# Kernel optimization log

Hardware: AMD Instinct MI355X
Metric: run time of the kernel (lower is better)

Reference implementation:

```python
import jax, jax.numpy as jnp
import numpy as np

N_NODES = 524288
N_EDGES = 2097152
B = 16384
CONCAT = 128 + 128 + 881  # 1137


def _glorot(key, shape):
    fan_in, fan_out = shape[0], shape[1]
    s = jnp.sqrt(6.0 / (fan_in + fan_out))
    return jax.random.uniform(key, shape, jnp.float32, -s, s)


def setup_inputs() -> dict:
    key = jax.random.key(0)
    ks = jax.random.split(key, 24)
    inp = {
        'drug_x': jax.random.normal(ks[0], (N_NODES, 30), jnp.float32),
        'edge_index': jax.random.randint(ks[1], (2, N_EDGES), 0, N_NODES, jnp.int32),
        'batch': jnp.sort(jax.random.randint(ks[2], (N_NODES,), 0, B, jnp.int32)),
        'protein_x': jax.random.normal(ks[3], (B, 979), jnp.float32),
        'fppubchem': jax.random.uniform(ks[4], (B, 881), jnp.float32),
        # GCN layers (PyG GCNConv: linear no-bias, bias added after aggregation)
        'W1': _glorot(ks[5], (30, 64)), 'b1': jnp.zeros((64,), jnp.float32),
        'W2': _glorot(ks[6], (64, 64)), 'b2': jnp.zeros((64,), jnp.float32),
        'W3': _glorot(ks[7], (64, 64)), 'b3': jnp.zeros((64,), jnp.float32),
        'fc_drug_w': _glorot(ks[8], (64, 128)), 'fc_drug_b': jnp.zeros((128,), jnp.float32),
        'fc_prot_w': _glorot(ks[9], (979, 128)), 'fc_prot_b': jnp.zeros((128,), jnp.float32),
        'fc1_w': _glorot(ks[10], (CONCAT, 512)), 'fc1_b': jnp.zeros((512,), jnp.float32),
        'fc2_w': _glorot(ks[11], (512, 256)), 'fc2_b': jnp.zeros((256,), jnp.float32),
        'fc3_w': _glorot(ks[12], (256, 1)), 'fc3_b': jnp.zeros((1,), jnp.float32),
    }
    return inp


def _gcn_layer(x, W, b, src, dst, deg_inv_sqrt, n_nodes):
    # x' = D^-1/2 (A+I) D^-1/2 (x W) + b   (src/dst already include self-loops)
    h = x @ W
    norm = deg_inv_sqrt[src] * deg_inv_sqrt[dst]  # [E+N]
    msg = h[src] * norm[:, None]
    out = jax.ops.segment_sum(msg, dst, num_segments=n_nodes)
    return out + b


def reference(drug_x, edge_index, batch, protein_x, fppubchem,
              W1, b1, W2, b2, W3, b3,
              fc_drug_w, fc_drug_b, fc_prot_w, fc_prot_b,
              fc1_w, fc1_b, fc2_w, fc2_b, fc3_w, fc3_b):
    n = drug_x.shape[0]
    loops = jnp.arange(n, dtype=edge_index.dtype)
    src = jnp.concatenate([edge_index[0], loops])
    dst = jnp.concatenate([edge_index[1], loops])
    deg = jax.ops.segment_sum(jnp.ones_like(src, jnp.float32), dst, num_segments=n)
    deg_inv_sqrt = jnp.where(deg > 0, jax.lax.rsqrt(jnp.maximum(deg, 1.0)), 0.0)

    h = jax.nn.relu(_gcn_layer(drug_x, W1, b1, src, dst, deg_inv_sqrt, n))
    h = jax.nn.relu(_gcn_layer(h, W2, b2, src, dst, deg_inv_sqrt, n))
    h = jax.nn.relu(_gcn_layer(h, W3, b3, src, dst, deg_inv_sqrt, n))

    # global mean pool over graphs
    nb = fppubchem.shape[0]
    sums = jax.ops.segment_sum(h, batch, num_segments=nb)
    cnts = jax.ops.segment_sum(jnp.ones((n,), jnp.float32), batch, num_segments=nb)
    pooled = sums / jnp.maximum(cnts, 1.0)[:, None]

    drug = jax.nn.relu(pooled @ fc_drug_w + fc_drug_b)
    prot = jax.nn.relu(protein_x @ fc_prot_w + fc_prot_b)
    comb = jnp.concatenate([drug, prot, fppubchem], axis=1)

    # fresh LayerNorm (weight=1, bias=0); dropout treated as identity (eval/deterministic)
    mu = jnp.mean(comb, axis=-1, keepdims=True)
    var = jnp.mean((comb - mu) ** 2, axis=-1, keepdims=True)
    comb = (comb - mu) * jax.lax.rsqrt(var + 1e-5)

    comb = jax.nn.relu(comb @ fc1_w + fc1_b)
    comb = jax.nn.relu(comb @ fc2_w + fc2_b)
    return comb @ fc3_w + fc3_b
```

## Files before the change

### kernel.cpp

```cpp
#include <hip/hip_runtime.h>
#include <hip/hip_bf16.h>

#define CONCAT_F 1137
#define CONCAT_P 1152
#define PROT_K 979
#define PROT_P 992

typedef __attribute__((ext_vector_type(8))) short bf16x8;
typedef __attribute__((ext_vector_type(4))) float f32x4;

static __device__ __forceinline__ float bfu2f(unsigned short u) {
  return __uint_as_float(((unsigned)u) << 16);
}
static __device__ __forceinline__ unsigned short f2bfu(float v) {
  __hip_bfloat16 t = __float2bfloat16(v);
  unsigned short u;
  __builtin_memcpy(&u, &t, 2);
  return u;
}

#define ACC4(A0, A1, A2, A3, U)        \
  {                                    \
    A0 += bfu2f((U).x & 0xffffu);      \
    A1 += bfu2f((U).x >> 16);          \
    A2 += bfu2f((U).y & 0xffffu);      \
    A3 += bfu2f((U).y >> 16);          \
  }

__global__ void k_count(const int* __restrict__ dst, int* __restrict__ rs, int E) {
  int e = blockIdx.x * blockDim.x + threadIdx.x;
  if (e < E) atomicAdd(&rs[dst[e]], 1);
}

__global__ void k_disk(const int* __restrict__ cnt, float* __restrict__ dis, int n) {
  int i = blockIdx.x * blockDim.x + threadIdx.x;
  if (i < n) dis[i] = rsqrtf(1.0f + (float)cnt[i]);
}

__global__ void k_scan_p1(const int* __restrict__ cnt, int* __restrict__ part, int n) {
  __shared__ int red[256];
  int tid = threadIdx.x;
  long base = (long)blockIdx.x * 1024 + tid * 4;
  int s = 0;
#pragma unroll
  for (int i = 0; i < 4; ++i) {
    long j = base + i;
    if (j < n) s += cnt[j];
  }
  red[tid] = s;
  __syncthreads();
  for (int off = 128; off; off >>= 1) {
    if (tid < off) red[tid] += red[tid + off];
    __syncthreads();
  }
  if (tid == 0) part[blockIdx.x] = red[0];
}

__global__ void k_scan_p2(int* __restrict__ part, int nb) {
  __shared__ int a[1024], b_[1024];
  int t = threadIdx.x;
  a[t] = (t < nb) ? part[t] : 0;
  __syncthreads();
  int* s = a;
  int* d = b_;
  for (int off = 1; off < 1024; off <<= 1) {
    d[t] = s[t] + ((t >= off) ? s[t - off] : 0);
    __syncthreads();
    int* tmp = s;
    s = d;
    d = tmp;
  }
  if (t < nb) part[t] = (t == 0) ? 0 : s[t - 1];
}

__global__ void k_scan_p3(int* __restrict__ rs, const int* __restrict__ part, int n) {
  __shared__ int a[256], b_[256];
  int tid = threadIdx.x;
  long base = (long)blockIdx.x * 1024 + tid * 4;
  int v[4];
#pragma unroll
  for (int i = 0; i < 4; ++i) {
    long j = base + i;
    v[i] = (j < n) ? rs[j] : 0;
  }
  a[tid] = v[0] + v[1] + v[2] + v[3];
  __syncthreads();
  int* s = a;
  int* d = b_;
  for (int off = 1; off < 256; off <<= 1) {
    d[tid] = s[tid] + ((tid >= off) ? s[tid - off] : 0);
    __syncthreads();
    int* t2 = s;
    s = d;
    d = t2;
  }
  int run = part[blockIdx.x] + ((tid == 0) ? 0 : s[tid - 1]);
#pragma unroll
  for (int i = 0; i < 4; ++i) {
    long j = base + i;
    if (j < n) {
      rs[j] = run;
      run += v[i];
    }
  }
}

__global__ void k_scatter(const int* __restrict__ src, const int* __restrict__ dst,
                          int* __restrict__ rs, int* __restrict__ csr, int E) {
  int e = blockIdx.x * blockDim.x + threadIdx.x;
  if (e < E) {
    int pos = atomicAdd(&rs[dst[e]], 1);
    __builtin_nontemporal_store(src[e], &csr[pos]);
  }
}

template <int K, bool ACT>
__global__ __launch_bounds__(256) void k_mm(const void* __restrict__ Xv,
                                            const float* __restrict__ W,
                                            const float* __restrict__ bprev,
                                            const float* __restrict__ dis,
                                            unsigned short* __restrict__ M, int n) {
  __shared__ __align__(16) float hT[K][68];
  __shared__ __align__(16) float Ws[K * 64];
  __shared__ float disS[64];
  int tid = threadIdx.x;
  int rb = blockIdx.x * 64;
  for (int j = tid; j < K * 16; j += 256) ((float4*)Ws)[j] = ((const float4*)W)[j];
  if (tid < 64) disS[tid] = (rb + tid < n) ? dis[rb + tid] : 0.0f;
  __syncthreads();
  if constexpr (ACT) {
    const unsigned short* X = (const unsigned short*)Xv;
    int k = tid & 63;
    float bk = bprev[k];
#pragma unroll
    for (int r = tid >> 6; r < 64; r += 4) {
      float h = 0.0f;
      if (rb + r < n) {
        float raw = bfu2f(X[(long)(rb + r) * 64 + k]);
        h = fmaxf(fmaf(raw, disS[r], bk), 0.0f);
      }
      hT[k][r] = h;
    }
  } else {
    const float* X = (const float*)Xv;
    for (int idx = tid; idx < 64 * K; idx += 256) {
      int r = idx / K, k = idx - r * K;
      hT[k][r] = (rb + r < n) ? X[(long)(rb + r) * K + k] : 0.0f;
    }
  }
  __syncthreads();
  int rt = (tid & 15) * 4;
  int ct = (tid >> 4) * 4;
  float acc[4][4] = {};
#pragma unroll 5
  for (int k = 0; k < K; ++k) {
    float4 xr = *(const float4*)&hT[k][rt];
    float4 wr = *(const float4*)&Ws[k * 64 + ct];
    float xa[4] = {xr.x, xr.y, xr.z, xr.w};
    float wa[4] = {wr.x, wr.y, wr.z, wr.w};
#pragma unroll
    for (int i = 0; i < 4; ++i)
#pragma unroll
      for (int j = 0; j < 4; ++j) acc[i][j] = fmaf(xa[i], wa[j], acc[i][j]);
  }
#pragma unroll
  for (int i = 0; i < 4; ++i) {
    int row = rb + rt + i;
    if (row >= n) break;
    float dv = disS[rt + i];
    ushort4 pk;
    pk.x = f2bfu(acc[i][0] * dv);
    pk.y = f2bfu(acc[i][1] * dv);
    pk.z = f2bfu(acc[i][2] * dv);
    pk.w = f2bfu(acc[i][3] * dv);
    *(ushort4*)&M[(long)row * 64 + ct] = pk;
  }
}

static __device__ __forceinline__ void gather_rows(
    const int* __restrict__ rs, const int* __restrict__ csr,
    const unsigned short* __restrict__ Min, int node, int l16,
    float& A0, float& A1, float& A2, float& A3) {
  float a0, a1, a2, a3;
  float b0 = 0.f, b1 = 0.f, b2 = 0.f, b3 = 0.f;
  float c0 = 0.f, c1 = 0.f, c2 = 0.f, c3 = 0.f;
  float d0 = 0.f, d1 = 0.f, d2 = 0.f, d3 = 0.f;
  uint2 v = *(const uint2*)(Min + (size_t)node * 64 + l16 * 4);
  a0 = bfu2f(v.x & 0xffffu);
  a1 = bfu2f(v.x >> 16);
  a2 = bfu2f(v.y & 0xffffu);
  a3 = bfu2f(v.y >> 16);
  int start = (node == 0) ? 0 : rs[node - 1];
  int end = rs[node];
  int j = start;
  for (; j + 3 < end; j += 4) {
    int s0 = csr[j], s1 = csr[j + 1], s2 = csr[j + 2], s3 = csr[j + 3];
    uint2 u0 = *(const uint2*)(Min + (size_t)s0 * 64 + l16 * 4);
    uint2 u1 = *(const uint2*)(Min + (size_t)s1 * 64 + l16 * 4);
    uint2 u2 = *(const uint2*)(Min + (size_t)s2 * 64 + l16 * 4);
    uint2 u3 = *(const uint2*)(Min + (size_t)s3 * 64 + l16 * 4);
    ACC4(a0, a1, a2, a3, u0);
    ACC4(b0, b1, b2, b3, u1);
    ACC4(c0, c1, c2, c3, u2);
    ACC4(d0, d1, d2, d3, u3);
  }
  if (j + 1 < end) {
    int s0 = csr[j], s1 = csr[j + 1];
    uint2 u0 = *(const uint2*)(Min + (size_t)s0 * 64 + l16 * 4);
    uint2 u1 = *(const uint2*)(Min + (size_t)s1 * 64 + l16 * 4);
    ACC4(a0, a1, a2, a3, u0);
    ACC4(b0, b1, b2, b3, u1);
    j += 2;
  }
  if (j < end) {
    uint2 u0 = *(const uint2*)(Min + (size_t)csr[j] * 64 + l16 * 4);
    ACC4(a0, a1, a2, a3, u0);
  }
  A0 = (a0 + b0) + (c0 + d0);
  A1 = (a1 + b1) + (c1 + d1);
  A2 = (a2 + b2) + (c2 + d2);
  A3 = (a3 + b3) + (c3 + d3);
}

__global__ __launch_bounds__(256) void k_gmm(
    const int* __restrict__ rs, const int* __restrict__ csr,
    const unsigned short* __restrict__ Min, const float* __restrict__ dis,
    const float* __restrict__ bias, const float* __restrict__ W,
    unsigned short* __restrict__ Mout, int n) {
  __shared__ __align__(16) unsigned short As[64 * 64];
  __shared__ __align__(16) unsigned short Bt[64 * 64];
  const int tid = threadIdx.x;
  const int bm = blockIdx.x * 64;
  {
    int nn = tid & 63, k0 = (tid >> 6) * 16;
    bf16x8 v0, v1;
#pragma unroll
    for (int i = 0; i < 8; ++i) v0[i] = (short)f2bfu(W[(size_t)(k0 + i) * 64 + nn]);
#pragma unroll
    for (int i = 0; i < 8; ++i) v1[i] = (short)f2bfu(W[(size_t)(k0 + 8 + i) * 64 + nn]);
    int off0 = (nn * 128 + k0 * 2) ^ ((nn & 7) << 4);
    int off1 = (nn * 128 + (k0 + 8) * 2) ^ ((nn & 7) << 4);
    *(bf16x8*)((char*)Bt + off0) = v0;
    *(bf16x8*)((char*)Bt + off1) = v1;
  }
  const int lane = tid & 63;
  const int wv = tid >> 6;
  const int grp = lane >> 4, l16 = lane & 15;
  const float4 bb = *(const float4*)(bias + l16 * 4);
  for (int p = 0; p < 4; ++p) {
    int local = wv * 16 + p * 4 + grp;
    int node = bm + local;
    float A0 = 0.f, A1 = 0.f, A2 = 0.f, A3 = 0.f, dv = 0.f;
    if (node < n) {
      gather_rows(rs, csr, Min, node, l16, A0, A1, A2, A3);
      dv = dis[node];
    }
    ushort4 h;
    h.x = f2bfu(fmaxf(fmaf(A0, dv, bb.x), 0.f));
    h.y = f2bfu(fmaxf(fmaf(A1, dv, bb.y), 0.f));
    h.z = f2bfu(fmaxf(fmaf(A2, dv, bb.z), 0.f));
    h.w = f2bfu(fmaxf(fmaf(A3, dv, bb.w), 0.f));
    int off = (local * 128 + l16 * 8) ^ ((local & 7) << 4);
    *(ushort4*)((char*)As + off) = h;
  }
  __syncthreads();
  const int kb = lane >> 4, fr = lane & 15;
  f32x4 acc[4];
#pragma unroll
  for (int i = 0; i < 4; ++i) acc[i] = f32x4{0.f, 0.f, 0.f, 0.f};
  const int ar = wv * 16 + fr;
#pragma unroll
  for (int kc = 0; kc < 2; ++kc) {
    int aoff = (ar * 128 + kc * 64 + kb * 16) ^ ((ar & 7) << 4);
    bf16x8 a = *(const bf16x8*)((char*)As + aoff);
#pragma unroll
    for (int ni = 0; ni < 4; ++ni) {
      int nr = ni * 16 + fr;
      int boff = (nr * 128 + kc * 64 + kb * 16) ^ ((nr & 7) << 4);
      bf16x8 b = *(const bf16x8*)((char*)Bt + boff);
      acc[ni] = __builtin_amdgcn_mfma_f32_16x16x32_bf16(a, b, acc[ni], 0, 0, 0);
    }
  }
#pragma unroll
  for (int r = 0; r < 4; ++r) {
    int row = bm + wv * 16 + kb * 4 + r;
    if (row < n) {
      float dvo = dis[row];
#pragma unroll
      for (int ni = 0; ni < 4; ++ni)
        Mout[(size_t)row * 64 + ni * 16 + fr] = f2bfu(acc[ni][r] * dvo);
    }
  }
}

__global__ void k_gather_act(const int* __restrict__ rs, const int* __restrict__ csr,
                             const unsigned short* __restrict__ M,
                             const float* __restrict__ dis, const float* __restrict__ bias,
                             unsigned short* __restrict__ H, int n) {
  int w = (int)((blockIdx.x * (long)blockDim.x + threadIdx.x) >> 6);
  int lane = threadIdx.x & 63;
  int grp = lane >> 4, l16 = lane & 15;
  int node = w * 4 + grp;
  if (node >= n) return;
  float A0, A1, A2, A3;
  gather_rows(rs, csr, M, node, l16, A0, A1, A2, A3);
  float dv = dis[node];
  float4 bb = *(const float4*)(bias + l16 * 4);
  ushort4 o;
  o.x = f2bfu(fmaxf(fmaf(A0, dv, bb.x), 0.f));
  o.y = f2bfu(fmaxf(fmaf(A1, dv, bb.y), 0.f));
  o.z = f2bfu(fmaxf(fmaf(A2, dv, bb.z), 0.f));
  o.w = f2bfu(fmaxf(fmaf(A3, dv, bb.w), 0.f));
  *(ushort4*)(H + (size_t)node * 64 + l16 * 4) = o;
}

__global__ void k_pool8(const unsigned short* __restrict__ H, const int* __restrict__ batch,
                        float* __restrict__ sums, float* __restrict__ cntf, int n) {
  int w = (int)((blockIdx.x * (long)blockDim.x + threadIdx.x) >> 6);
  int lane = threadIdx.x & 63;
  int r0 = w * 8;
  if (r0 >= n) return;
  int cur = batch[r0];
  float acc = bfu2f(H[(long)r0 * 64 + lane]);
  float c = 1.0f;
  for (int i = 1; i < 8; ++i) {
    int r = r0 + i;
    if (r >= n) break;
    int b = batch[r];
    float v = bfu2f(H[(long)r * 64 + lane]);
    if (b == cur) {
      acc += v;
      c += 1.0f;
    } else {
      unsafeAtomicAdd(&sums[(long)cur * 64 + lane], acc);
      if (lane == 0) unsafeAtomicAdd(&cntf[cur], c);
      cur = b;
      acc = v;
      c = 1.0f;
    }
  }
  unsafeAtomicAdd(&sums[(long)cur * 64 + lane], acc);
  if (lane == 0) unsafeAtomicAdd(&cntf[cur], c);
}

__global__ void k_drugfc(const float* __restrict__ sums, const float* __restrict__ cnt,
                         const float* __restrict__ W, const float* __restrict__ b,
                         float* __restrict__ out, int B) {
  __shared__ float ps[64];
  int row = blockIdx.x;
  int tid = threadIdx.x;
  float inv = 1.0f / fmaxf(cnt[row], 1.0f);
  if (tid < 64) ps[tid] = sums[(long)row * 64 + tid] * inv;
  __syncthreads();
  float acc = b[tid];
#pragma unroll 8
  for (int k = 0; k < 64; ++k) acc = fmaf(ps[k], W[k * 128 + tid], acc);
  out[(long)row * 128 + tid] = fmaxf(acc, 0.0f);
}

__global__ void k_cvt_bf16(const float* __restrict__ X, unsigned short* __restrict__ Y,
                           int Kin, int ldout) {
  int row = blockIdx.x;
  const float* xr = X + (size_t)row * Kin;
  unsigned short* yr = Y + (size_t)row * ldout;
  for (int j = threadIdx.x; j < ldout; j += 256)
    yr[j] = (j < Kin) ? f2bfu(xr[j]) : 0;
}

template <bool SPLIT, typename OT>
__global__ __launch_bounds__(256, 3) void k_gemm2(
    const unsigned short* __restrict__ A, const float* __restrict__ W,
    const float* __restrict__ bias, OT* __restrict__ C,
    int Mrows, int N, int K, int lda, int nsteps, int chunkSteps) {
  __shared__ __align__(16) unsigned short As[2][64 * 32];
  __shared__ __align__(16) unsigned short Bs[2][128 * 32];
  const int tid = threadIdx.x;
  const int lane = tid & 63;
  const int wid = tid >> 6;
  const int bm = blockIdx.x * 64;
  const int bn = blockIdx.y * 128;
  const int kb = lane >> 4, fr = lane & 15;
  const int ss0 = blockIdx.z * chunkSteps;
  const int ss1 = min(nsteps, ss0 + chunkSteps);

  f32x4 acc[8];
#pragma unroll
  for (int j = 0; j < 8; ++j) acc[j] = f32x4{0.f, 0.f, 0.f, 0.f};

  const int ar = wid * 16 + fr;
  const int aOff = (ar * 64 + kb * 16) ^ ((ar & 7) << 4);
  int bOff[8];
#pragma unroll
  for (int ni = 0; ni < 8; ++ni) {
    int nr = ni * 16 + fr;
    bOff[ni] = (nr * 64 + kb * 16) ^ ((nr & 7) << 4);
  }
  const int arow = tid >> 2, ac = tid & 3;
  const int aW = (arow * 64 + ac * 16) ^ ((arow & 7) << 4);
  const int bn_ = tid & 127, bk0 = (tid >> 7) * 2;
  int bW[2];
#pragma unroll
  for (int p = 0; p < 2; ++p) {
    int kbb = bk0 + p;
    bW[p] = (bn_ * 64 + kbb * 16) ^ ((bn_ & 7) << 4);
  }

  bf16x8 pa;
  float pb[2][8];
  const unsigned short* aptr = A + (size_t)(bm + arow) * lda + ac * 8;

#define LOAD_STEP(S)                                              \
  {                                                               \
    int k0 = (S) * 32;                                            \
    pa = *(const bf16x8*)(aptr + k0);                             \
    _Pragma("unroll") for (int p = 0; p < 2; ++p) {               \
      _Pragma("unroll") for (int i = 0; i < 8; ++i) {             \
        int gk = k0 + (bk0 + p) * 8 + i;                          \
        pb[p][i] = (gk < K) ? W[(size_t)gk * N + bn + bn_] : 0.f; \
      }                                                           \
    }                                                             \
  }
#define STORE_STEP(BUF)                                           \
  {                                                               \
    *(bf16x8*)((char*)As[BUF] + aW) = pa;                         \
    _Pragma("unroll") for (int p = 0; p < 2; ++p) {               \
      bf16x8 v;                                                   \
      _Pragma("unroll") for (int i = 0; i < 8; ++i)               \
          v[i] = (short)f2bfu(pb[p][i]);                          \
      *(bf16x8*)((char*)Bs[BUF] + bW[p]) = v;                     \
    }                                                             \
  }

  LOAD_STEP(ss0);
  STORE_STEP(0);
  __syncthreads();
  int cur = 0;
  for (int s = ss0; s < ss1; ++s) {
    bool more = (s + 1 < ss1);
    if (more) LOAD_STEP(s + 1);
    bf16x8 a0 = *(const bf16x8*)((char*)As[cur] + aOff);
#pragma unroll
    for (int ni = 0; ni < 8; ++ni) {
      bf16x8 b = *(const bf16x8*)((char*)Bs[cur] + bOff[ni]);
      acc[ni] = __builtin_amdgcn_mfma_f32_16x16x32_bf16(a0, b, acc[ni], 0, 0, 0);
    }
    if (more) {
      STORE_STEP(cur ^ 1);
      __syncthreads();
      cur ^= 1;
    }
  }
  if constexpr (SPLIT) {
    float* Cz = (float*)C + (size_t)blockIdx.z * Mrows * N;
#pragma unroll
    for (int ni = 0; ni < 8; ++ni)
#pragma unroll
      for (int r = 0; r < 4; ++r) {
        int row = bm + wid * 16 + kb * 4 + r;
        int col = bn + ni * 16 + fr;
        Cz[(size_t)row * N + col] = acc[ni][r];
      }
  } else {
    float bv[8];
#pragma unroll
    for (int ni = 0; ni < 8; ++ni) bv[ni] = bias[bn + ni * 16 + fr];
#pragma unroll
    for (int ni = 0; ni < 8; ++ni)
#pragma unroll
      for (int r = 0; r < 4; ++r) {
        int row = bm + wid * 16 + kb * 4 + r;
        int col = bn + ni * 16 + fr;
        float x = fmaxf(acc[ni][r] + bv[ni], 0.f);
        if constexpr (__hip_internal::is_same<OT, float>::value) {
          C[(size_t)row * N + col] = x;
        } else {
          C[(size_t)row * N + col] = f2bfu(x);
        }
      }
  }
#undef LOAD_STEP
#undef STORE_STEP
}

__global__ void k_concat_ln(const float* __restrict__ drug, const float* __restrict__ protP,
                            const float* __restrict__ bp, const float* __restrict__ fpp,
                            unsigned short* __restrict__ comb, int B) {
  __shared__ float buf[CONCAT_F];
  __shared__ float rs[4], rs2[4];
  int row = blockIdx.x;
  int tid = threadIdx.x;
  const size_t MN = (size_t)B * 128;
  float s = 0.0f, s2 = 0.0f;
  for (int j = tid; j < CONCAT_F; j += 256) {
    float v;
    if (j < 128) {
      v = drug[(long)row * 128 + j];
    } else if (j < 256) {
      int c = j - 128;
      size_t o = (size_t)row * 128 + c;
      float acc = protP[o] + protP[MN + o] + protP[2 * MN + o] + protP[3 * MN + o];
      v = fmaxf(acc + bp[c], 0.0f);
    } else {
      v = fpp[(long)row * 881 + (j - 256)];
    }
    buf[j] = v;
    s += v;
    s2 += v * v;
  }
  for (int o = 32; o; o >>= 1) {
    s += __shfl_down(s, o, 64);
    s2 += __shfl_down(s2, o, 64);
  }
  int lane = tid & 63, wid = tid >> 6;
  if (lane == 0) { rs[wid] = s; rs2[wid] = s2; }
  __syncthreads();
  if (tid == 0) {
    float ts = rs[0] + rs[1] + rs[2] + rs[3];
    float ts2 = rs2[0] + rs2[1] + rs2[2] + rs2[3];
    float mu = ts / (float)CONCAT_F;
    float var = ts2 / (float)CONCAT_F - mu * mu;
    rs[0] = mu;
    rs2[0] = rsqrtf(fmaxf(var, 0.0f) + 1e-5f);
  }
  __syncthreads();
  float mu = rs[0], inv = rs2[0];
  for (int j = tid; j < CONCAT_P; j += 256) {
    unsigned short o = (j < CONCAT_F) ? f2bfu((buf[j] - mu) * inv) : 0;
    comb[(long)row * CONCAT_P + j] = o;
  }
}

__global__ void k_fc3(const float* __restrict__ X, const float* __restrict__ W,
                      const float* __restrict__ bias, float* __restrict__ out, int B) {
  int w = (int)((blockIdx.x * (long)blockDim.x + threadIdx.x) >> 6);
  int lane = threadIdx.x & 63;
  if (w >= B) return;
  float s = 0.0f;
#pragma unroll
  for (int j = 0; j < 4; ++j) s = fmaf(X[(long)w * 256 + lane + j * 64], W[lane + j * 64], s);
  for (int o = 32; o; o >>= 1) s += __shfl_down(s, o, 64);
  if (lane == 0) out[w] = s + bias[0];
}

extern "C" void kernel_launch(void* const* d_in, const int* in_sizes, int n_in,
                              void* d_out, int out_size, void* d_ws, size_t ws_size,
                              hipStream_t stream) {
  const float* drug_x = (const float*)d_in[0];
  const int* ei = (const int*)d_in[1];
  const int* batch = (const int*)d_in[2];
  const float* protein_x = (const float*)d_in[3];
  const float* fpp = (const float*)d_in[4];
  const float* W1 = (const float*)d_in[5];
  const float* b1 = (const float*)d_in[6];
  const float* W2 = (const float*)d_in[7];
  const float* b2 = (const float*)d_in[8];
  const float* W3 = (const float*)d_in[9];
  const float* b3 = (const float*)d_in[10];
  const float* Wd = (const float*)d_in[11];
  const float* bd = (const float*)d_in[12];
  const float* Wp = (const float*)d_in[13];
  const float* bp = (const float*)d_in[14];
  const float* Wf1 = (const float*)d_in[15];
  const float* bf1 = (const float*)d_in[16];
  const float* Wf2 = (const float*)d_in[17];
  const float* bf2 = (const float*)d_in[18];
  const float* Wf3 = (const float*)d_in[19];
  const float* bf3 = (const float*)d_in[20];
  float* out = (float*)d_out;

  const int N = in_sizes[0] / 30;
  const int E = in_sizes[1] / 2;
  const int B = in_sizes[4] / 881;

  int* rs = (int*)d_ws;
  float* dis = (float*)d_ws + ((size_t)N + 1);
  int* csr = (int*)d_ws + (2 * (size_t)N + 1);
  size_t oM = 2 * (size_t)N + 2 + (size_t)E;
  unsigned short* M = (unsigned short*)((float*)d_ws + oM);
  unsigned short* H = M + (size_t)N * 64;
  float* sums = (float*)d_ws + (oM + 64 * (size_t)N);
  float* cntf = sums + (size_t)B * 64;
  int* part = (int*)(cntf + B);
  unsigned short* protbh = (unsigned short*)(part + 1024);
  float* tail = (float*)d_ws;
  float* drug = tail;
  float* protP = drug + (size_t)B * 128;
  unsigned short* combh = (unsigned short*)(protP + 4 * (size_t)B * 128);
  unsigned short* act1h = combh + (size_t)B * CONCAT_P;
  float* act2 = (float*)(act1h + (size_t)B * 512);

  const int* srcIdx = ei;
  const int* dstIdx = ei + E;

  k_cvt_bf16<<<B, 256, 0, stream>>>(protein_x, protbh, PROT_K, PROT_P);

  hipMemsetAsync(rs, 0, ((size_t)N + 1) * sizeof(int), stream);
  k_count<<<(E + 255) / 256, 256, 0, stream>>>(dstIdx, rs, E);
  k_disk<<<(N + 255) / 256, 256, 0, stream>>>(rs, dis, N);
  int NB = (N + 1023) / 1024;
  k_scan_p1<<<NB, 256, 0, stream>>>(rs, part, N);
  k_scan_p2<<<1, 1024, 0, stream>>>(part, NB);
  k_scan_p3<<<NB, 256, 0, stream>>>(rs, part, N);
  k_scatter<<<(E + 255) / 256, 256, 0, stream>>>(srcIdx, dstIdx, rs, csr, E);

  int mmBlocks = (N + 63) / 64;
  int gWaves = (N + 3) / 4;
  int gBlocks = (gWaves + 3) / 4;
  k_mm<30, false><<<mmBlocks, 256, 0, stream>>>(drug_x, W1, nullptr, dis, M, N);
  k_gmm<<<mmBlocks, 256, 0, stream>>>(rs, csr, M, dis, b1, W2, H, N);
  k_gmm<<<mmBlocks, 256, 0, stream>>>(rs, csr, H, dis, b2, W3, M, N);
  k_gather_act<<<gBlocks, 256, 0, stream>>>(rs, csr, M, dis, b3, H, N);

  hipMemsetAsync(sums, 0, ((size_t)B * 64 + B) * sizeof(float), stream);
  int poolWaves = (N + 7) / 8;
  k_pool8<<<(poolWaves + 3) / 4, 256, 0, stream>>>(H, batch, sums, cntf, N);

  k_drugfc<<<B, 128, 0, stream>>>(sums, cntf, Wd, bd, drug, B);
  k_gemm2<true, float><<<dim3(B / 64, 1, 4), 256, 0, stream>>>(
      protbh, Wp, nullptr, protP, B, 128, PROT_K, PROT_P, 31, 8);
  k_concat_ln<<<B, 256, 0, stream>>>(drug, protP, bp, fpp, combh, B);
  k_gemm2<false, unsigned short><<<dim3(B / 64, 4, 1), 256, 0, stream>>>(
      combh, Wf1, bf1, act1h, B, 512, CONCAT_F, CONCAT_P, 36, 36);
  k_gemm2<false, float><<<dim3(B / 64, 2, 1), 256, 0, stream>>>(
      act1h, Wf2, bf2, act2, B, 256, 512, 512, 16, 16);
  k_fc3<<<(B + 3) / 4, 256, 0, stream>>>(act2, Wf3, bf3, out, B);
}
```

Baseline: 880.9 us.

## Build CSR via two-level bucket sort to localize degree and scatter atomics

```diff
diff --git a/kernel.cpp b/kernel.cpp
--- a/kernel.cpp
+++ b/kernel.cpp
@@ -27,39 +27,21 @@
     A3 += bfu2f((U).y >> 16);          \
   }
 
-__global__ void k_count(const int* __restrict__ dst, int* __restrict__ rs, int E) {
+__global__ void k_bcount(const int* __restrict__ dst, int* __restrict__ bkt, int E) {
   int e = blockIdx.x * blockDim.x + threadIdx.x;
-  if (e < E) atomicAdd(&rs[dst[e]], 1);
-}
-
-__global__ void k_disk(const int* __restrict__ cnt, float* __restrict__ dis, int n) {
-  int i = blockIdx.x * blockDim.x + threadIdx.x;
-  if (i < n) dis[i] = rsqrtf(1.0f + (float)cnt[i]);
-}
-
-__global__ void k_scan_p1(const int* __restrict__ cnt, int* __restrict__ part, int n) {
-  __shared__ int red[256];
-  int tid = threadIdx.x;
-  long base = (long)blockIdx.x * 1024 + tid * 4;
-  int s = 0;
-#pragma unroll
-  for (int i = 0; i < 4; ++i) {
-    long j = base + i;
-    if (j < n) s += cnt[j];
-  }
-  red[tid] = s;
-  __syncthreads();
-  for (int off = 128; off; off >>= 1) {
-    if (tid < off) red[tid] += red[tid + off];
-    __syncthreads();
-  }
-  if (tid == 0) part[blockIdx.x] = red[0];
-}
-
-__global__ void k_scan_p2(int* __restrict__ part, int nb) {
+  if (e < E) atomicAdd(&bkt[(dst[e] >> 10) * 8 + (blockIdx.x & 7)], 1);
+}
+
+__global__ void k_bscan(int* __restrict__ bkt, int total) {
   __shared__ int a[1024], b_[1024];
   int t = threadIdx.x;
-  a[t] = (t < nb) ? part[t] : 0;
+  int base = t * 4;
+  int v0 = 0, v1 = 0, v2 = 0, v3 = 0;
+  if (base + 0 < total) v0 = bkt[base + 0];
+  if (base + 1 < total) v1 = bkt[base + 1];
+  if (base + 2 < total) v2 = bkt[base + 2];
+  if (base + 3 < total) v3 = bkt[base + 3];
+  a[t] = v0 + v1 + v2 + v3;
   __syncthreads();
   int* s = a;
   int* d = b_;
@@ -70,6 +52,82 @@
     s = d;
     d = tmp;
   }
+  int run = (t == 0) ? 0 : s[t - 1];
+  if (base + 0 < total) { bkt[base + 0] = run; run += v0; }
+  if (base + 1 < total) { bkt[base + 1] = run; run += v1; }
+  if (base + 2 < total) { bkt[base + 2] = run; run += v2; }
+  if (base + 3 < total) { bkt[base + 3] = run; run += v3; }
+}
+
+__global__ void k_bscatter(const int* __restrict__ src, const int* __restrict__ dst,
+                           int* __restrict__ bkt, int2* __restrict__ pairs, int E) {
+  int e = blockIdx.x * blockDim.x + threadIdx.x;
+  if (e < E) {
+    int d = dst[e];
+    int pos = atomicAdd(&bkt[(d >> 10) * 8 + (blockIdx.x & 7)], 1);
+    pairs[pos] = make_int2(src[e], d);
+  }
+}
+
+__global__ void k_pcount(const int2* __restrict__ pairs, const int* __restrict__ bkt,
+                         int* __restrict__ rs) {
+  int b = blockIdx.x;
+  int start = (b == 0) ? 0 : bkt[b * 8 - 1];
+  int end = bkt[b * 8 + 7];
+  for (int e = start + threadIdx.x; e < end; e += blockDim.x)
+    atomicAdd(&rs[pairs[e].y], 1);
+}
+
+__global__ void k_scatter2(const int2* __restrict__ pairs, const int* __restrict__ bkt,
+                           int* __restrict__ rs, int* __restrict__ csr) {
+  int b = blockIdx.x;
+  int start = (b == 0) ? 0 : bkt[b * 8 - 1];
+  int end = bkt[b * 8 + 7];
+  for (int e = start + threadIdx.x; e < end; e += blockDim.x) {
+    int2 p = pairs[e];
+    int pos = atomicAdd(&rs[p.y], 1);
+    csr[pos] = p.x;
+  }
+}
+
+__global__ void k_disk(const int* __restrict__ cnt, float* __restrict__ dis, int n) {
+  int i = blockIdx.x * blockDim.x + threadIdx.x;
+  if (i < n) dis[i] = rsqrtf(1.0f + (float)cnt[i]);
+}
+
+__global__ void k_scan_p1(const int* __restrict__ cnt, int* __restrict__ part, int n) {
+  __shared__ int red[256];
+  int tid = threadIdx.x;
+  long base = (long)blockIdx.x * 1024 + tid * 4;
+  int s = 0;
+#pragma unroll
+  for (int i = 0; i < 4; ++i) {
+    long j = base + i;
+    if (j < n) s += cnt[j];
+  }
+  red[tid] = s;
+  __syncthreads();
+  for (int off = 128; off; off >>= 1) {
+    if (tid < off) red[tid] += red[tid + off];
+    __syncthreads();
+  }
+  if (tid == 0) part[blockIdx.x] = red[0];
+}
+
+__global__ void k_scan_p2(int* __restrict__ part, int nb) {
+  __shared__ int a[1024], b_[1024];
+  int t = threadIdx.x;
+  a[t] = (t < nb) ? part[t] : 0;
+  __syncthreads();
+  int* s = a;
+  int* d = b_;
+  for (int off = 1; off < 1024; off <<= 1) {
+    d[t] = s[t] + ((t >= off) ? s[t - off] : 0);
+    __syncthreads();
+    int* tmp = s;
+    s = d;
+    d = tmp;
+  }
   if (t < nb) part[t] = (t == 0) ? 0 : s[t - 1];
 }
 
@@ -102,15 +160,6 @@
       rs[j] = run;
       run += v[i];
     }
-  }
-}
-
-__global__ void k_scatter(const int* __restrict__ src, const int* __restrict__ dst,
-                          int* __restrict__ rs, int* __restrict__ csr, int E) {
-  int e = blockIdx.x * blockDim.x + threadIdx.x;
-  if (e < E) {
-    int pos = atomicAdd(&rs[dst[e]], 1);
-    __builtin_nontemporal_store(src[e], &csr[pos]);
   }
 }
 
@@ -581,7 +630,9 @@
   float* sums = (float*)d_ws + (oM + 64 * (size_t)N);
   float* cntf = sums + (size_t)B * 64;
   int* part = (int*)(cntf + B);
-  unsigned short* protbh = (unsigned short*)(part + 1024);
+  int* bkt = part + 1024;
+  unsigned short* protbh = (unsigned short*)(bkt + 4096);
+  int2* pairs = (int2*)H;
   float* tail = (float*)d_ws;
   float* drug = tail;
   float* protP = drug + (size_t)B * 128;
@@ -594,14 +645,20 @@
 
   k_cvt_bf16<<<B, 256, 0, stream>>>(protein_x, protbh, PROT_K, PROT_P);
 
+  const int NBUK = (N + 1023) >> 10;
   hipMemsetAsync(rs, 0, ((size_t)N + 1) * sizeof(int), stream);
-  k_count<<<(E + 255) / 256, 256, 0, stream>>>(dstIdx, rs, E);
+  hipMemsetAsync(bkt, 0, (size_t)NBUK * 8 * sizeof(int), stream);
+  int EB = (E + 255) / 256;
+  k_bcount<<<EB, 256, 0, stream>>>(dstIdx, bkt, E);
+  k_bscan<<<1, 1024, 0, stream>>>(bkt, NBUK * 8);
+  k_bscatter<<<EB, 256, 0, stream>>>(srcIdx, dstIdx, bkt, pairs, E);
+  k_pcount<<<NBUK, 256, 0, stream>>>(pairs, bkt, rs);
   k_disk<<<(N + 255) / 256, 256, 0, stream>>>(rs, dis, N);
   int NB = (N + 1023) / 1024;
   k_scan_p1<<<NB, 256, 0, stream>>>(rs, part, N);
   k_scan_p2<<<1, 1024, 0, stream>>>(part, NB);
   k_scan_p3<<<NB, 256, 0, stream>>>(rs, part, N);
-  k_scatter<<<(E + 255) / 256, 256, 0, stream>>>(srcIdx, dstIdx, rs, csr, E);
+  k_scatter2<<<NBUK, 256, 0, stream>>>(pairs, bkt, rs, csr);
 
   int mmBlocks = (N + 63) / 64;
   int gWaves = (N + 3) / 4;
```

Measured after the change: 1.053 ms. 1.19x slower.

## Merge degree-norm into scan and fuse scatter, first matmul, protein cast

Applied to the files above, without the earlier changes.

```diff
diff --git a/kernel.cpp b/kernel.cpp
--- a/kernel.cpp
+++ b/kernel.cpp
@@ -32,12 +32,8 @@
   if (e < E) atomicAdd(&rs[dst[e]], 1);
 }
 
-__global__ void k_disk(const int* __restrict__ cnt, float* __restrict__ dis, int n) {
-  int i = blockIdx.x * blockDim.x + threadIdx.x;
-  if (i < n) dis[i] = rsqrtf(1.0f + (float)cnt[i]);
-}
-
-__global__ void k_scan_p1(const int* __restrict__ cnt, int* __restrict__ part, int n) {
+__global__ void k_scan_p1(const int* __restrict__ cnt, int* __restrict__ part,
+                          float* __restrict__ dis, int n) {
   __shared__ int red[256];
   int tid = threadIdx.x;
   long base = (long)blockIdx.x * 1024 + tid * 4;
@@ -45,7 +41,11 @@
 #pragma unroll
   for (int i = 0; i < 4; ++i) {
     long j = base + i;
-    if (j < n) s += cnt[j];
+    if (j < n) {
+      int c = cnt[j];
+      s += c;
+      dis[j] = rsqrtf(1.0f + (float)c);
+    }
   }
   red[tid] = s;
   __syncthreads();
@@ -105,75 +105,71 @@
   }
 }
 
-__global__ void k_scatter(const int* __restrict__ src, const int* __restrict__ dst,
-                          int* __restrict__ rs, int* __restrict__ csr, int E) {
-  int e = blockIdx.x * blockDim.x + threadIdx.x;
-  if (e < E) {
-    int pos = atomicAdd(&rs[dst[e]], 1);
-    __builtin_nontemporal_store(src[e], &csr[pos]);
-  }
-}
-
-template <int K, bool ACT>
-__global__ __launch_bounds__(256) void k_mm(const void* __restrict__ Xv,
-                                            const float* __restrict__ W,
-                                            const float* __restrict__ bprev,
-                                            const float* __restrict__ dis,
-                                            unsigned short* __restrict__ M, int n) {
-  __shared__ __align__(16) float hT[K][68];
-  __shared__ __align__(16) float Ws[K * 64];
+__global__ __launch_bounds__(256) void k_fat(
+    const int* __restrict__ src, const int* __restrict__ dst,
+    int* __restrict__ rs, int* __restrict__ csr, int E, int EB,
+    const float* __restrict__ X, const float* __restrict__ W1,
+    const float* __restrict__ dis, unsigned short* __restrict__ M, int n, int mmB,
+    const float* __restrict__ PX, unsigned short* __restrict__ PY) {
+  __shared__ __align__(16) float hT[30][68];
+  __shared__ __align__(16) float Ws[30 * 64];
   __shared__ float disS[64];
+  int bx = blockIdx.x;
   int tid = threadIdx.x;
-  int rb = blockIdx.x * 64;
-  for (int j = tid; j < K * 16; j += 256) ((float4*)Ws)[j] = ((const float4*)W)[j];
-  if (tid < 64) disS[tid] = (rb + tid < n) ? dis[rb + tid] : 0.0f;
-  __syncthreads();
-  if constexpr (ACT) {
-    const unsigned short* X = (const unsigned short*)Xv;
-    int k = tid & 63;
-    float bk = bprev[k];
-#pragma unroll
-    for (int r = tid >> 6; r < 64; r += 4) {
-      float h = 0.0f;
-      if (rb + r < n) {
-        float raw = bfu2f(X[(long)(rb + r) * 64 + k]);
-        h = fmaxf(fmaf(raw, disS[r], bk), 0.0f);
-      }
-      hT[k][r] = h;
-    }
-  } else {
-    const float* X = (const float*)Xv;
+  if (bx < EB) {
+    int e = bx * 256 + tid;
+    if (e < E) {
+      int pos = atomicAdd(&rs[dst[e]], 1);
+      __builtin_nontemporal_store(src[e], &csr[pos]);
+    }
+    return;
+  }
+  bx -= EB;
+  if (bx < mmB) {
+    const int K = 30;
+    int rb = bx * 64;
+    for (int j = tid; j < K * 16; j += 256) ((float4*)Ws)[j] = ((const float4*)W1)[j];
+    if (tid < 64) disS[tid] = (rb + tid < n) ? dis[rb + tid] : 0.0f;
+    __syncthreads();
     for (int idx = tid; idx < 64 * K; idx += 256) {
       int r = idx / K, k = idx - r * K;
       hT[k][r] = (rb + r < n) ? X[(long)(rb + r) * K + k] : 0.0f;
     }
-  }
-  __syncthreads();
-  int rt = (tid & 15) * 4;
-  int ct = (tid >> 4) * 4;
-  float acc[4][4] = {};
+    __syncthreads();
+    int rt = (tid & 15) * 4;
+    int ct = (tid >> 4) * 4;
+    float acc[4][4] = {};
 #pragma unroll 5
-  for (int k = 0; k < K; ++k) {
-    float4 xr = *(const float4*)&hT[k][rt];
-    float4 wr = *(const float4*)&Ws[k * 64 + ct];
-    float xa[4] = {xr.x, xr.y, xr.z, xr.w};
-    float wa[4] = {wr.x, wr.y, wr.z, wr.w};
-#pragma unroll
-    for (int i = 0; i < 4; ++i)
-#pragma unroll
-      for (int j = 0; j < 4; ++j) acc[i][j] = fmaf(xa[i], wa[j], acc[i][j]);
-  }
-#pragma unroll
-  for (int i = 0; i < 4; ++i) {
-    int row = rb + rt + i;
-    if (row >= n) break;
-    float dv = disS[rt + i];
-    ushort4 pk;
-    pk.x = f2bfu(acc[i][0] * dv);
-    pk.y = f2bfu(acc[i][1] * dv);
-    pk.z = f2bfu(acc[i][2] * dv);
-    pk.w = f2bfu(acc[i][3] * dv);
-    *(ushort4*)&M[(long)row * 64 + ct] = pk;
+    for (int k = 0; k < K; ++k) {
+      float4 xr = *(const float4*)&hT[k][rt];
+      float4 wr = *(const float4*)&Ws[k * 64 + ct];
+      float xa[4] = {xr.x, xr.y, xr.z, xr.w};
+      float wa[4] = {wr.x, wr.y, wr.z, wr.w};
+#pragma unroll
+      for (int i = 0; i < 4; ++i)
+#pragma unroll
+        for (int j = 0; j < 4; ++j) acc[i][j] = fmaf(xa[i], wa[j], acc[i][j]);
+    }
+#pragma unroll
+    for (int i = 0; i < 4; ++i) {
+      int row = rb + rt + i;
+      if (row >= n) break;
+      float dv = disS[rt + i];
+      ushort4 pk;
+      pk.x = f2bfu(acc[i][0] * dv);
+      pk.y = f2bfu(acc[i][1] * dv);
+      pk.z = f2bfu(acc[i][2] * dv);
+      pk.w = f2bfu(acc[i][3] * dv);
+      *(ushort4*)&M[(long)row * 64 + ct] = pk;
+    }
+    return;
+  }
+  bx -= mmB;
+  {
+    const float* xr = PX + (size_t)bx * PROT_K;
+    unsigned short* yr = PY + (size_t)bx * PROT_P;
+    for (int j = tid; j < PROT_P; j += 256)
+      yr[j] = (j < PROT_K) ? f2bfu(xr[j]) : 0;
   }
 }
 
@@ -358,15 +354,6 @@
   out[(long)row * 128 + tid] = fmaxf(acc, 0.0f);
 }
 
-__global__ void k_cvt_bf16(const float* __restrict__ X, unsigned short* __restrict__ Y,
-                           int Kin, int ldout) {
-  int row = blockIdx.x;
-  const float* xr = X + (size_t)row * Kin;
-  unsigned short* yr = Y + (size_t)row * ldout;
-  for (int j = threadIdx.x; j < ldout; j += 256)
-    yr[j] = (j < Kin) ? f2bfu(xr[j]) : 0;
-}
-
 template <bool SPLIT, typename OT>
 __global__ __launch_bounds__(256, 3) void k_gemm2(
     const unsigned short* __restrict__ A, const float* __restrict__ W,
@@ -592,21 +579,22 @@
   const int* srcIdx = ei;
   const int* dstIdx = ei + E;
 
-  k_cvt_bf16<<<B, 256, 0, stream>>>(protein_x, protbh, PROT_K, PROT_P);
-
   hipMemsetAsync(rs, 0, ((size_t)N + 1) * sizeof(int), stream);
   k_count<<<(E + 255) / 256, 256, 0, stream>>>(dstIdx, rs, E);
-  k_disk<<<(N + 255) / 256, 256, 0, stream>>>(rs, dis, N);
   int NB = (N + 1023) / 1024;
-  k_scan_p1<<<NB, 256, 0, stream>>>(rs, part, N);
+  k_scan_p1<<<NB, 256, 0, stream>>>(rs, part, dis, N);
   k_scan_p2<<<1, 1024, 0, stream>>>(part, NB);
   k_scan_p3<<<NB, 256, 0, stream>>>(rs, part, N);
-  k_scatter<<<(E + 255) / 256, 256, 0, stream>>>(srcIdx, dstIdx, rs, csr, E);
-
+
+  int EB = (E + 255) / 256;
   int mmBlocks = (N + 63) / 64;
+  k_fat<<<EB + mmBlocks + B, 256, 0, stream>>>(
+      srcIdx, dstIdx, rs, csr, E, EB,
+      drug_x, W1, dis, M, N, mmBlocks,
+      protein_x, protbh);
+
   int gWaves = (N + 3) / 4;
   int gBlocks = (gWaves + 3) / 4;
-  k_mm<30, false><<<mmBlocks, 256, 0, stream>>>(drug_x, W1, nullptr, dis, M, N);
   k_gmm<<<mmBlocks, 256, 0, stream>>>(rs, csr, M, dis, b1, W2, H, N);
   k_gmm<<<mmBlocks, 256, 0, stream>>>(rs, csr, H, dis, b2, W3, M, N);
   k_gather_act<<<gBlocks, 256, 0, stream>>>(rs, csr, M, dis, b3, H, N);
```

Result: no change. 884.7 us (+0.4%).

## Partition CSR count and scatter atomics by destination range per XCD

Applied to the files above, without the earlier changes.

```diff
diff --git a/kernel.cpp b/kernel.cpp
--- a/kernel.cpp
+++ b/kernel.cpp
@@ -27,17 +27,36 @@
     A3 += bfu2f((U).y >> 16);          \
   }
 
-__global__ void k_count(const int* __restrict__ dst, int* __restrict__ rs, int E) {
-  int e = blockIdx.x * blockDim.x + threadIdx.x;
-  if (e < E) atomicAdd(&rs[dst[e]], 1);
-}
-
-__global__ void k_disk(const int* __restrict__ cnt, float* __restrict__ dis, int n) {
-  int i = blockIdx.x * blockDim.x + threadIdx.x;
-  if (i < n) dis[i] = rsqrtf(1.0f + (float)cnt[i]);
-}
-
-__global__ void k_scan_p1(const int* __restrict__ cnt, int* __restrict__ part, int n) {
+__global__ void k_count_xcd(const int* __restrict__ dst, int* __restrict__ rs,
+                            int E, int shift, int chunk) {
+  int cls = blockIdx.x & 7;
+  int slice = blockIdx.x >> 3;
+  int s0 = slice * chunk;
+  int s1 = min(E, s0 + chunk);
+  for (int e = s0 + threadIdx.x; e < s1; e += blockDim.x) {
+    int d = dst[e];
+    if ((d >> shift) == cls) atomicAdd(&rs[d], 1);
+  }
+}
+
+__global__ void k_scatter_xcd(const int* __restrict__ src, const int* __restrict__ dst,
+                              int* __restrict__ rs, int* __restrict__ csr,
+                              int E, int shift, int chunk) {
+  int cls = blockIdx.x & 7;
+  int slice = blockIdx.x >> 3;
+  int s0 = slice * chunk;
+  int s1 = min(E, s0 + chunk);
+  for (int e = s0 + threadIdx.x; e < s1; e += blockDim.x) {
+    int d = dst[e];
+    if ((d >> shift) == cls) {
+      int pos = atomicAdd(&rs[d], 1);
+      csr[pos] = src[e];
+    }
+  }
+}
+
+__global__ void k_scan_p1(const int* __restrict__ cnt, int* __restrict__ part,
+                          float* __restrict__ dis, int n) {
   __shared__ int red[256];
   int tid = threadIdx.x;
   long base = (long)blockIdx.x * 1024 + tid * 4;
@@ -45,7 +64,11 @@
 #pragma unroll
   for (int i = 0; i < 4; ++i) {
     long j = base + i;
-    if (j < n) s += cnt[j];
+    if (j < n) {
+      int c = cnt[j];
+      s += c;
+      dis[j] = rsqrtf(1.0f + (float)c);
+    }
   }
   red[tid] = s;
   __syncthreads();
@@ -102,15 +125,6 @@
       rs[j] = run;
       run += v[i];
     }
-  }
-}
-
-__global__ void k_scatter(const int* __restrict__ src, const int* __restrict__ dst,
-                          int* __restrict__ rs, int* __restrict__ csr, int E) {
-  int e = blockIdx.x * blockDim.x + threadIdx.x;
-  if (e < E) {
-    int pos = atomicAdd(&rs[dst[e]], 1);
-    __builtin_nontemporal_store(src[e], &csr[pos]);
   }
 }
 
@@ -592,16 +606,20 @@
   const int* srcIdx = ei;
   const int* dstIdx = ei + E;
 
+  int shift = 0;
+  while (((N - 1) >> shift) > 7) ++shift;
+  const int CHUNK = 2048;
+  int G = (E + CHUNK - 1) / CHUNK;
+
   k_cvt_bf16<<<B, 256, 0, stream>>>(protein_x, protbh, PROT_K, PROT_P);
 
   hipMemsetAsync(rs, 0, ((size_t)N + 1) * sizeof(int), stream);
-  k_count<<<(E + 255) / 256, 256, 0, stream>>>(dstIdx, rs, E);
-  k_disk<<<(N + 255) / 256, 256, 0, stream>>>(rs, dis, N);
+  k_count_xcd<<<8 * G, 256, 0, stream>>>(dstIdx, rs, E, shift, CHUNK);
   int NB = (N + 1023) / 1024;
-  k_scan_p1<<<NB, 256, 0, stream>>>(rs, part, N);
+  k_scan_p1<<<NB, 256, 0, stream>>>(rs, part, dis, N);
   k_scan_p2<<<1, 1024, 0, stream>>>(part, NB);
   k_scan_p3<<<NB, 256, 0, stream>>>(rs, part, N);
-  k_scatter<<<(E + 255) / 256, 256, 0, stream>>>(srcIdx, dstIdx, rs, csr, E);
+  k_scatter_xcd<<<8 * G, 256, 0, stream>>>(srcIdx, dstIdx, rs, csr, E, shift, CHUNK);
 
   int mmBlocks = (N + 63) / 64;
   int gWaves = (N + 3) / 4;
```

After: 792.8 us. 1.11x faster.
